# Kernel optimization log

Measured on AMD Instinct MI355X. Metric: run time of the kernel, lower is better.

Reference implementation:

```python
import jax, jax.numpy as jnp
import numpy as np

B, H, W, C = 8, 64, 64, 128
BN_EPS = 1e-3  # keras BatchNormalization default epsilon


def setup_inputs() -> dict:
    key = jax.random.key(0)
    ks = jax.random.split(key, 8)
    scale = 1.0 / np.sqrt(C)
    return {
        "x": jax.random.normal(ks[0], (B, H, W, C), dtype=jnp.float32),
        "wq": jax.random.normal(ks[1], (C, C), dtype=jnp.float32) * scale,
        "bq": jnp.zeros((C,), dtype=jnp.float32),
        "wk": jax.random.normal(ks[2], (C, C), dtype=jnp.float32) * scale,
        "bk": jnp.zeros((C,), dtype=jnp.float32),
        "wv": jax.random.normal(ks[3], (C, C), dtype=jnp.float32) * scale,
        "bv": jnp.zeros((C,), dtype=jnp.float32),
        "gamma": jnp.ones((C,), dtype=jnp.float32),
        "beta": jnp.zeros((C,), dtype=jnp.float32),
        "mov_mean": jax.random.normal(ks[4], (C,), dtype=jnp.float32) * 0.1,
        "mov_var": jax.random.uniform(ks[5], (C,), dtype=jnp.float32) * 0.5 + 0.5,
    }


def reference(x, wq, bq, wk, bk, wv, bv, gamma, beta, mov_mean, mov_var):
    b, h, w, c = x.shape
    n = h * w
    # 1x1 convs == per-pixel linear projections
    q = (jnp.einsum('bhwc,cd->bhwd', x, wq) + bq).reshape(b, n, c)
    k = (jnp.einsum('bhwc,cd->bhwd', x, wk) + bk).reshape(b, n, c)
    v = (jnp.einsum('bhwc,cd->bhwd', x, wv) + bv).reshape(b, n, c)
    # full [n, n] attention matrix (as in the original module)
    scores = jnp.einsum('bnc,bmc->bnm', q, k) / jnp.sqrt(jnp.asarray(c, x.dtype))
    attn = jax.nn.softmax(scores, axis=-1)  # dropout is identity in inference
    out = jnp.einsum('bnm,bmc->bnc', attn, v).reshape(b, h, w, c)
    out = out + x  # residual
    # BatchNormalization, inference mode (moving statistics)
    inv = gamma * jax.lax.rsqrt(mov_var + BN_EPS)
    out = out * inv + (beta - mov_mean * inv)
    return out
```

## Files before the change

### kernel.cpp

```cpp
#include <hip/hip_runtime.h>


typedef __attribute__((ext_vector_type(8))) short bf16x8;
typedef __attribute__((ext_vector_type(4))) float f32x4;

__device__ __forceinline__ unsigned short f2bf(float f) {
  unsigned int u = __builtin_bit_cast(unsigned int, f);
  u += 0x7fffu + ((u >> 16) & 1u);
  return (unsigned short)(u >> 16);
}
__device__ __forceinline__ unsigned int pack2(float a, float b) {
  return (unsigned int)f2bf(a) | ((unsigned int)f2bf(b) << 16);
}
__device__ __forceinline__ unsigned int pack2t(float a, float b) {
  return (__builtin_bit_cast(unsigned int, a) >> 16) |
         (__builtin_bit_cast(unsigned int, b) & 0xFFFF0000u);
}
__device__ __forceinline__ float fexp2(float x) {
  return __builtin_amdgcn_exp2f(x);
}

__device__ __forceinline__ void dma16(const void* g, void* l) {
  __builtin_amdgcn_global_load_lds(
      (const __attribute__((address_space(1))) unsigned int*)g,
      (__attribute__((address_space(3))) unsigned int*)l, 16, 0, 0);
}

#define SCALE_Q (0.08838834764831845f * 1.44269504088896340f)

__global__ void prep_wt(const float* __restrict__ wq, const float* __restrict__ wk,
                        const float* __restrict__ wv, unsigned short* __restrict__ wt) {
  const float* W = (blockIdx.x == 0) ? wq : (blockIdx.x == 1 ? wk : wv);
  const float sc = (blockIdx.x == 0) ? SCALE_Q : 1.0f;
  unsigned short* out = wt + blockIdx.x * 16384;
  int id = blockIdx.y * 256 + threadIdx.x;
  int n  = id >> 5;
  int kb = (id & 31) * 4;
#pragma unroll
  for (int k = 0; k < 4; ++k)
    out[n * 128 + kb + k] = f2bf(W[(kb + k) * 128 + n] * sc);
}

__global__ __launch_bounds__(256) void qkv_proj(
    const float* __restrict__ x, const unsigned short* __restrict__ wt,
    const float* __restrict__ bq, const float* __restrict__ bk, const float* __restrict__ bv,
    unsigned short* __restrict__ Qg, unsigned short* __restrict__ Kg,
    unsigned short* __restrict__ Vtg) {
  __shared__ unsigned short xs[64 * 128];
  __shared__ unsigned short obuf[9216];
  const int t = threadIdx.x;
  const int p = blockIdx.y;
  const int rowblk = blockIdx.x * 64;

#pragma unroll
  for (int i = 0; i < 8; ++i) {
    int flat = t * 4 + i * 1024;
    int row = flat >> 7, col = flat & 127;
    float4 v = *(const float4*)(x + (size_t)(rowblk + row) * 128 + col);
    unsigned int u0 = pack2(v.x, v.y), u1 = pack2(v.z, v.w);
    int pos = (col >> 3) ^ (row & 15);
    *(uint2*)(xs + row * 128 + pos * 8 + (col & 7)) = make_uint2(u0, u1);
  }
  __syncthreads();

  const int lane = t & 63, wv_ = t >> 6;
  const int lm = lane & 15, quad = lane >> 4;

  bf16x8 a[4];
  {
    int row = wv_ * 16 + lm;
#pragma unroll
    for (int ks = 0; ks < 4; ++ks)
      a[ks] = __builtin_bit_cast(bf16x8,
          *(const uint4*)(xs + row * 128 + (((ks * 4 + quad) ^ lm) * 8)));
  }

  const unsigned short* w = wt + p * 16384;
  const float* bias = (p == 0) ? bq : (p == 1 ? bk : bv);
  const float bsc = (p == 0) ? SCALE_Q : 1.0f;

  const f32x4 zero4 = {0.f, 0.f, 0.f, 0.f};
  f32x4 acc[8];
#pragma unroll
  for (int ct = 0; ct < 8; ++ct) acc[ct] = zero4;

#pragma unroll
  for (int ct = 0; ct < 8; ++ct) {
    int n = ct * 16 + lm;
    const uint4* wp = (const uint4*)(w + n * 128 + quad * 8);
#pragma unroll
    for (int ks = 0; ks < 4; ++ks) {
      bf16x8 bfr = __builtin_bit_cast(bf16x8, wp[ks * 4]);
      acc[ct] = __builtin_amdgcn_mfma_f32_16x16x32_bf16(a[ks], bfr, acc[ct], 0, 0, 0);
    }
  }

  const int b   = rowblk >> 12;
  const int nb0 = rowblk & 4095;

  if (p < 2) {
    int rowb = wv_ * 16 + quad * 4;
#pragma unroll
    for (int ct = 0; ct < 8; ++ct) {
      int c = ct * 16 + lm;
      float bb = bias[c] * bsc;
#pragma unroll
      for (int r = 0; r < 4; ++r)
        obuf[(rowb + r) * 136 + c] = f2bf(acc[ct][r] + bb);
    }
    __syncthreads();
    unsigned short* og = (p == 0) ? Qg : Kg;
    int row = t >> 2;
#pragma unroll
    for (int j = 0; j < 4; ++j) {
      int ch = (t & 3) * 4 + j;
      int pos = (p == 1) ? (ch ^ (row & 15)) : ch;
      uint4 vv = *(const uint4*)(obuf + row * 136 + ch * 8);
      *(uint4*)(og + (size_t)(rowblk + row) * 128 + pos * 8) = vv;
    }
  } else {
    int key_base = wv_ * 16 + quad * 4;
#pragma unroll
    for (int ct = 0; ct < 8; ++ct) {
      int c = ct * 16 + lm;
      float bb = bias[c];
      unsigned int u0 = pack2(acc[ct][0] + bb, acc[ct][1] + bb);
      unsigned int u1 = pack2(acc[ct][2] + bb, acc[ct][3] + bb);
      *(uint2*)(obuf + c * 72 + key_base) = make_uint2(u0, u1);
    }
    __syncthreads();
    int d = t >> 1;
#pragma unroll
    for (int j = 0; j < 4; ++j) {
      int ch = (t & 1) * 4 + j;
      uint4 vv = *(const uint4*)(obuf + d * 72 + ch * 8);
      *(uint4*)(Vtg + (size_t)b * 524288 + (size_t)d * 4096 + nb0 + ch * 8) = vv;
    }
  }
}

__global__ __launch_bounds__(256, 2) void flash_attn(
    const unsigned short* __restrict__ Qg, const unsigned short* __restrict__ Kg,
    const unsigned short* __restrict__ Vtg, const float* __restrict__ x,
    const float* __restrict__ gamma, const float* __restrict__ beta,
    const float* __restrict__ mmean, const float* __restrict__ mvar,
    float* __restrict__ out) {
  __shared__ unsigned short Kt[2][16384];
  __shared__ unsigned short Pbuf[8192];

  const int b  = blockIdx.x & 7;
  const int qt = blockIdx.x >> 3;
  const int t = threadIdx.x;
  const int lane = t & 63;
  const int w = t >> 6;
  const int lm = lane & 15, quad = lane >> 4;
  const int q0 = qt * 64;

  const unsigned short* Qb = Qg  + (size_t)b * 524288;
  const unsigned short* Kb = Kg  + (size_t)b * 524288;
  const unsigned short* Vb = Vtg + (size_t)b * 524288;

  bf16x8 qf[4][4];
#pragma unroll
  for (int nt = 0; nt < 4; ++nt) {
    const uint4* qp = (const uint4*)(Qb + (size_t)(q0 + nt * 16 + lm) * 128 + quad * 8);
#pragma unroll
    for (int ks = 0; ks < 4; ++ks) qf[nt][ks] = __builtin_bit_cast(bf16x8, qp[ks * 4]);
  }

  const f32x4 zero4 = {0.f, 0.f, 0.f, 0.f};
  f32x4 o[2][4];
#pragma unroll
  for (int mt = 0; mt < 2; ++mt)
#pragma unroll
    for (int nt = 0; nt < 4; ++nt) o[mt][nt] = zero4;
  float lp[4] = {0.f, 0.f, 0.f, 0.f};

  {
    const unsigned short* src = Kb + (size_t)w * 4096 + lane * 8;
    unsigned short* dst = &Kt[0][w * 4096];
#pragma unroll
    for (int j = 0; j < 8; ++j) dma16(src + j * 512, dst + j * 512);
  }
  __syncthreads();

#pragma unroll 1
  for (int kt = 0; kt < 32; ++kt) {
    const int bi = kt & 1;
    const int key0 = kt * 128;

    bf16x8 vf[2][4];
#pragma unroll
    for (int mt = 0; mt < 2; ++mt) {
      const uint4* vp = (const uint4*)(Vb + (size_t)(w * 32 + mt * 16 + lm) * 4096 + key0 + quad * 8);
#pragma unroll
      for (int ks = 0; ks < 4; ++ks) vf[mt][ks] = __builtin_bit_cast(bf16x8, vp[ks * 4]);
    }

    f32x4 sa[2][4];
#pragma unroll
    for (int mt = 0; mt < 2; ++mt)
#pragma unroll
      for (int nt = 0; nt < 4; ++nt) sa[mt][nt] = zero4;
#pragma unroll
    for (int mt = 0; mt < 2; ++mt) {
      const unsigned short* kr = &Kt[bi][(w * 32 + mt * 16 + lm) * 128];
      bf16x8 kf[4];
#pragma unroll
      for (int ks = 0; ks < 4; ++ks)
        kf[ks] = __builtin_bit_cast(bf16x8, *(const uint4*)(kr + ((ks * 4 + quad) ^ lm) * 8));
#pragma unroll
      for (int ks = 0; ks < 4; ++ks)
#pragma unroll
        for (int nt = 0; nt < 4; ++nt)
          sa[mt][nt] = __builtin_amdgcn_mfma_f32_16x16x32_bf16(kf[ks], qf[nt][ks], sa[mt][nt], 0, 0, 0);
    }

    {
      unsigned short* Ps = Pbuf;
      const int sub = (quad & 1) * 4;
#pragma unroll
      for (int mt = 0; mt < 2; ++mt) {
        int c16 = w * 4 + mt * 2 + (quad >> 1);
        int pos = c16 ^ lm;
#pragma unroll
        for (int nt = 0; nt < 4; ++nt) {
          float e0 = fexp2(sa[mt][nt][0]), e1 = fexp2(sa[mt][nt][1]);
          float e2 = fexp2(sa[mt][nt][2]), e3 = fexp2(sa[mt][nt][3]);
          lp[nt] += (e0 + e1) + (e2 + e3);
          *(uint2*)(Ps + (nt * 16 + lm) * 128 + pos * 8 + sub) =
              make_uint2(pack2t(e0, e1), pack2t(e2, e3));
        }
      }
    }
    __syncthreads();

    if (kt + 1 < 32) {
      const unsigned short* src = Kb + (size_t)(kt + 1) * 16384 + w * 4096 + lane * 8;
      unsigned short* dst = &Kt[bi ^ 1][w * 4096];
#pragma unroll
      for (int j = 0; j < 8; ++j) dma16(src + j * 512, dst + j * 512);
    }

    {
      const uint4* Pr = (const uint4*)Pbuf;
#pragma unroll
      for (int nt = 0; nt < 4; ++nt) {
        bf16x8 pf[4];
#pragma unroll
        for (int ks = 0; ks < 4; ++ks)
          pf[ks] = __builtin_bit_cast(bf16x8, Pr[(nt * 16 + lm) * 16 + ((ks * 4 + quad) ^ lm)]);
#pragma unroll
        for (int ks = 0; ks < 4; ++ks)
#pragma unroll
          for (int mt = 0; mt < 2; ++mt)
            o[mt][nt] = __builtin_amdgcn_mfma_f32_16x16x32_bf16(vf[mt][ks], pf[ks], o[mt][nt], 0, 0, 0);
      }
    }
    __syncthreads();
  }

  float* lred = (float*)Pbuf;
#pragma unroll
  for (int nt = 0; nt < 4; ++nt) {
    lp[nt] += __shfl_xor(lp[nt], 16);
    lp[nt] += __shfl_xor(lp[nt], 32);
  }
  if (quad == 0) {
#pragma unroll
    for (int nt = 0; nt < 4; ++nt) lred[w * 64 + nt * 16 + lm] = lp[nt];
  }
  __syncthreads();
  float rl[4];
#pragma unroll
  for (int nt = 0; nt < 4; ++nt) {
    int q = nt * 16 + lm;
    rl[nt] = 1.0f / ((lred[q] + lred[64 + q]) + (lred[128 + q] + lred[192 + q]));
  }

#pragma unroll
  for (int mt = 0; mt < 2; ++mt) {
    int c0 = w * 32 + mt * 16 + quad * 4;
    float4 gm = *(const float4*)(gamma + c0);
    float4 bt = *(const float4*)(beta + c0);
    float4 mm = *(const float4*)(mmean + c0);
    float4 mv = *(const float4*)(mvar + c0);
    float iv0 = gm.x * rsqrtf(mv.x + 1e-3f), iv1 = gm.y * rsqrtf(mv.y + 1e-3f);
    float iv2 = gm.z * rsqrtf(mv.z + 1e-3f), iv3 = gm.w * rsqrtf(mv.w + 1e-3f);
    float ad0 = bt.x - mm.x * iv0, ad1 = bt.y - mm.y * iv1;
    float ad2 = bt.z - mm.z * iv2, ad3 = bt.w - mm.w * iv3;
#pragma unroll
    for (int nt = 0; nt < 4; ++nt) {
      size_t g = ((size_t)b * 4096 + q0 + nt * 16 + lm) * 128 + c0;
      float4 xr = *(const float4*)(x + g);
      float4 ov;
      ov.x = (o[mt][nt][0] * rl[nt] + xr.x) * iv0 + ad0;
      ov.y = (o[mt][nt][1] * rl[nt] + xr.y) * iv1 + ad1;
      ov.z = (o[mt][nt][2] * rl[nt] + xr.z) * iv2 + ad2;
      ov.w = (o[mt][nt][3] * rl[nt] + xr.w) * iv3 + ad3;
      *(float4*)(out + g) = ov;
    }
  }
}

extern "C" void kernel_launch(void* const* d_in, const int* in_sizes, int n_in,
                              void* d_out, int out_size, void* d_ws, size_t ws_size,
                              hipStream_t stream) {
  const float* x     = (const float*)d_in[0];
  const float* wq    = (const float*)d_in[1];
  const float* bq    = (const float*)d_in[2];
  const float* wk    = (const float*)d_in[3];
  const float* bk    = (const float*)d_in[4];
  const float* wv    = (const float*)d_in[5];
  const float* bv    = (const float*)d_in[6];
  const float* gamma = (const float*)d_in[7];
  const float* beta  = (const float*)d_in[8];
  const float* mmean = (const float*)d_in[9];
  const float* mvar  = (const float*)d_in[10];
  float* out = (float*)d_out;

  unsigned short* wt  = (unsigned short*)d_ws;
  unsigned short* Qg  = wt + 3 * 128 * 128;
  unsigned short* Kg  = Qg + 8 * 4096 * 128;
  unsigned short* Vtg = Kg + 8 * 4096 * 128;

  prep_wt<<<dim3(3, 16), dim3(256), 0, stream>>>(wq, wk, wv, wt);
  qkv_proj<<<dim3(512, 3), dim3(256), 0, stream>>>(x, wt, bq, bk, bv, Qg, Kg, Vtg);
  flash_attn<<<dim3(512), dim3(256), 0, stream>>>(Qg, Kg, Vtg, x, gamma, beta,
                                                  mmean, mvar, out);
}
```

Before: 216.6 us.

## Software-pipeline flash attention: double-buffer P, single K buffer, one barrier per tile

Restructures the attention loop so the PV product for tile kt-1 runs after the QK/softmax of tile kt. P is double-buffered and K is single-buffered, and the two __syncthreads per iteration become one hand-written s_waitcnt+s_barrier. V fragments are loaded one iteration ahead, and manual vmcnt waits replace the compiler's synchronisation. This aims to cut barrier stalls and hide global-load latency. In exchange it relies on fragile inline waitcnt counts, which risk races if the counts are wrong.

```diff
diff --git a/kernel.cpp b/kernel.cpp
--- a/kernel.cpp
+++ b/kernel.cpp
@@ -139,14 +139,16 @@
   }
 }
 
-__global__ __launch_bounds__(256, 2) void flash_attn(
+__global__ __launch_bounds__(256)
+__attribute__((amdgpu_waves_per_eu(2, 2)))
+void flash_attn(
     const unsigned short* __restrict__ Qg, const unsigned short* __restrict__ Kg,
     const unsigned short* __restrict__ Vtg, const float* __restrict__ x,
     const float* __restrict__ gamma, const float* __restrict__ beta,
     const float* __restrict__ mmean, const float* __restrict__ mvar,
     float* __restrict__ out) {
-  __shared__ unsigned short Kt[2][16384];
-  __shared__ unsigned short Pbuf[8192];
+  __shared__ unsigned short Kt[16384];
+  __shared__ unsigned short Pbuf[2][8192];
 
   const int b  = blockIdx.x & 7;
   const int qt = blockIdx.x >> 3;
@@ -160,6 +162,13 @@
   const unsigned short* Kb = Kg  + (size_t)b * 524288;
   const unsigned short* Vb = Vtg + (size_t)b * 524288;
 
+  {
+    const unsigned short* src = Kb + (size_t)w * 4096 + lane * 8;
+    unsigned short* dst = &Kt[w * 4096];
+#pragma unroll
+    for (int j = 0; j < 8; ++j) dma16(src + j * 512, dst + j * 512);
+  }
+
   bf16x8 qf[4][4];
 #pragma unroll
   for (int nt = 0; nt < 4; ++nt) {
@@ -175,36 +184,22 @@
 #pragma unroll
     for (int nt = 0; nt < 4; ++nt) o[mt][nt] = zero4;
   float lp[4] = {0.f, 0.f, 0.f, 0.f};
-
-  {
-    const unsigned short* src = Kb + (size_t)w * 4096 + lane * 8;
-    unsigned short* dst = &Kt[0][w * 4096];
-#pragma unroll
-    for (int j = 0; j < 8; ++j) dma16(src + j * 512, dst + j * 512);
-  }
-  __syncthreads();
+  bf16x8 vf[2][4];
 
 #pragma unroll 1
   for (int kt = 0; kt < 32; ++kt) {
-    const int bi = kt & 1;
     const int key0 = kt * 128;
 
-    bf16x8 vf[2][4];
+    asm volatile("s_waitcnt vmcnt(8)" ::: "memory");
+
+    f32x4 sa[2][4];
+#pragma unroll
+    for (int mt = 0; mt < 2; ++mt)
+#pragma unroll
+      for (int nt = 0; nt < 4; ++nt) sa[mt][nt] = zero4;
 #pragma unroll
     for (int mt = 0; mt < 2; ++mt) {
-      const uint4* vp = (const uint4*)(Vb + (size_t)(w * 32 + mt * 16 + lm) * 4096 + key0 + quad * 8);
-#pragma unroll
-      for (int ks = 0; ks < 4; ++ks) vf[mt][ks] = __builtin_bit_cast(bf16x8, vp[ks * 4]);
-    }
-
-    f32x4 sa[2][4];
-#pragma unroll
-    for (int mt = 0; mt < 2; ++mt)
-#pragma unroll
-      for (int nt = 0; nt < 4; ++nt) sa[mt][nt] = zero4;
-#pragma unroll
-    for (int mt = 0; mt < 2; ++mt) {
-      const unsigned short* kr = &Kt[bi][(w * 32 + mt * 16 + lm) * 128];
+      const unsigned short* kr = &Kt[(w * 32 + mt * 16 + lm) * 128];
       bf16x8 kf[4];
 #pragma unroll
       for (int ks = 0; ks < 4; ++ks)
@@ -217,7 +212,7 @@
     }
 
     {
-      unsigned short* Ps = Pbuf;
+      unsigned short* Ps = Pbuf[kt & 1];
       const int sub = (quad & 1) * 4;
 #pragma unroll
       for (int mt = 0; mt < 2; ++mt) {
@@ -233,17 +228,17 @@
         }
       }
     }
-    __syncthreads();
-
+
+    asm volatile("s_waitcnt lgkmcnt(0)" ::: "memory");
     if (kt + 1 < 32) {
       const unsigned short* src = Kb + (size_t)(kt + 1) * 16384 + w * 4096 + lane * 8;
-      unsigned short* dst = &Kt[bi ^ 1][w * 4096];
+      unsigned short* dst = &Kt[w * 4096];
 #pragma unroll
       for (int j = 0; j < 8; ++j) dma16(src + j * 512, dst + j * 512);
     }
 
-    {
-      const uint4* Pr = (const uint4*)Pbuf;
+    if (kt > 0) {
+      const uint4* Pr = (const uint4*)Pbuf[(kt & 1) ^ 1];
 #pragma unroll
       for (int nt = 0; nt < 4; ++nt) {
         bf16x8 pf[4];
@@ -257,10 +252,34 @@
             o[mt][nt] = __builtin_amdgcn_mfma_f32_16x16x32_bf16(vf[mt][ks], pf[ks], o[mt][nt], 0, 0, 0);
       }
     }
-    __syncthreads();
-  }
-
-  float* lred = (float*)Pbuf;
+
+#pragma unroll
+    for (int mt = 0; mt < 2; ++mt) {
+      const uint4* vp = (const uint4*)(Vb + (size_t)(w * 32 + mt * 16 + lm) * 4096 + key0 + quad * 8);
+#pragma unroll
+      for (int ks = 0; ks < 4; ++ks) vf[mt][ks] = __builtin_bit_cast(bf16x8, vp[ks * 4]);
+    }
+
+    asm volatile("s_waitcnt lgkmcnt(0)\n\ts_barrier" ::: "memory");
+  }
+
+  {
+    const uint4* Pr = (const uint4*)Pbuf[1];
+#pragma unroll
+    for (int nt = 0; nt < 4; ++nt) {
+      bf16x8 pf[4];
+#pragma unroll
+      for (int ks = 0; ks < 4; ++ks)
+        pf[ks] = __builtin_bit_cast(bf16x8, Pr[(nt * 16 + lm) * 16 + ((ks * 4 + quad) ^ lm)]);
+#pragma unroll
+      for (int ks = 0; ks < 4; ++ks)
+#pragma unroll
+        for (int mt = 0; mt < 2; ++mt)
+          o[mt][nt] = __builtin_amdgcn_mfma_f32_16x16x32_bf16(vf[mt][ks], pf[ks], o[mt][nt], 0, 0, 0);
+    }
+  }
+
+  float* lred = (float*)Pbuf[0];
 #pragma unroll
   for (int nt = 0; nt < 4; ++nt) {
     lp[nt] += __shfl_xor(lp[nt], 16);
```

Result: faster. 207.1 us (-4.4%).
